# Kernel optimization log

Measured on AMD Instinct MI355X. Metric: run time of the kernel, lower is better.

## Reference

```python
import jax, jax.numpy as jnp
import numpy as np

B, K, D, H, NIRREPS = 1024, 16, 1024, 16, 16  # batch, seq_len(=group n), input_dim, heads, n_irreps
HD = D // H


def setup_inputs() -> dict:
    key = jax.random.key(0)
    ks = jax.random.split(key, 10)
    s = 1.0 / np.sqrt(D)
    return {
        "x": jax.random.normal(ks[0], (B, K, D), jnp.float32),
        "projectors": jax.random.normal(ks[1], (NIRREPS, K, K), jnp.float32) * 0.25,
        "Wq": jax.random.normal(ks[2], (D, D), jnp.float32) * s,
        "bq": jnp.zeros((D,), jnp.float32),
        "Wk": jax.random.normal(ks[3], (D, D), jnp.float32) * s,
        "bk": jnp.zeros((D,), jnp.float32),
        "Wv": jax.random.normal(ks[4], (D, D), jnp.float32) * s,
        "bv": jnp.zeros((D,), jnp.float32),
        "Wo": jax.random.normal(ks[5], (D, D), jnp.float32) * s,
        "bo": jnp.zeros((D,), jnp.float32),
    }


def reference(x, projectors, Wq, bq, Wk, bk, Wv, bv, Wo, bo):
    b, k, d = x.shape
    hd = d // H
    # QKV projections -> [b, H, k, hd]
    def heads(t):
        return t.reshape(b, k, H, hd).transpose(0, 2, 1, 3)
    Q = heads(x @ Wq + bq)
    Kt = heads(x @ Wk + bk)
    V = heads(x @ Wv + bv)
    scale = jnp.asarray(1.0 / np.sqrt(hd), x.dtype)

    # Per-irrep: project Q/K/V along the seq axis with P, run masked-free softmax
    # attention on tiny k x k scores, accumulate over irreps (eval mode, no dropout).
    def body(acc, P):
        Qp = jnp.einsum('ij,bhjd->bhid', P, Q)
        Kp = jnp.einsum('ij,bhjd->bhid', P, Kt)
        Vp = jnp.einsum('ij,bhjd->bhid', P, V)
        scores = jnp.einsum('bhid,bhjd->bhij', Qp, Kp) * scale
        w = jax.nn.softmax(scores, axis=-1)
        return acc + jnp.einsum('bhij,bhjd->bhid', w, Vp), None

    total, _ = jax.lax.scan(body, jnp.zeros_like(V), projectors)
    # merge heads -> [b, k, d], then output projection
    out = total.transpose(0, 2, 1, 3).reshape(b, k, d) @ Wo + bo
    return out
```

## Files before the change

### kernel.cpp

```cpp
#include <hip/hip_runtime.h>


typedef unsigned short u16;
typedef unsigned int u32;
typedef __attribute__((ext_vector_type(8))) __bf16 bf16x8;
typedef __attribute__((ext_vector_type(4))) float f32x4;
typedef __attribute__((ext_vector_type(4))) u32 u32x4;
typedef __attribute__((ext_vector_type(4))) u16 u16x4;
typedef __attribute__((address_space(1))) void gvoid;
typedef __attribute__((address_space(3))) void svoid;

#define MFMA16(a, b, c) __builtin_amdgcn_mfma_f32_16x16x32_bf16(a, b, c, 0, 0, 0)

__device__ __forceinline__ u16 f2bf(float f) {
  u32 u = __builtin_bit_cast(u32, f);
  return (u16)((u + 0x7fffu + ((u >> 16) & 1u)) >> 16);
}
__device__ __forceinline__ float bf2f(u16 h) {
  u32 u = ((u32)h) << 16;
  return __builtin_bit_cast(float, u);
}
__device__ __forceinline__ bf16x8 ld_frag(const u16* p) {
  u32x4 v = *reinterpret_cast<const u32x4*>(p);
  return __builtin_bit_cast(bf16x8, v);
}
__device__ __forceinline__ bf16x8 ld_frag_lo(const u16* p, int lane) {
  u32x4 v = {0u, 0u, 0u, 0u};
  if (lane < 32) v = *reinterpret_cast<const u32x4*>(p);
  return __builtin_bit_cast(bf16x8, v);
}
__device__ __forceinline__ void async16(const u16* g, u16* l) {
  __builtin_amdgcn_global_load_lds((gvoid*)g, (svoid*)l, 16, 0, 0);
}
__device__ __forceinline__ void lds_fence() {
  asm volatile("s_waitcnt lgkmcnt(0)" ::: "memory");
}

__global__ __launch_bounds__(256) void detect_dtype(const u32* __restrict__ x,
                                                    int* __restrict__ flag) {
  const int tid = threadIdx.x;
  int cnt = 0;
  for (int i = tid; i < 16384; i += 256) {
    const u32 e = (x[i] >> 23) & 0xffu;
    cnt += (e >= 64u && e <= 191u) ? 1 : 0;
  }
  __shared__ int sred[4];
  for (int o = 32; o; o >>= 1) cnt += __shfl_down(cnt, o);
  if ((tid & 63) == 0) sred[tid >> 6] = cnt;
  __syncthreads();
  if (tid == 0)
    flag[0] = (sred[0] + sred[1] + sred[2] + sred[3] > 8192) ? 1 : 0;
}

__global__ __launch_bounds__(256) void convert_bf16(const void* __restrict__ src,
                                                    u16* __restrict__ dst, int n,
                                                    const int* __restrict__ flag) {
  const int isf32 = *flag;
  const int base = (blockIdx.x * 256 + threadIdx.x) * 8;
  if (base >= n) return;
  if (isf32) {
    const float* s = (const float*)src;
#pragma unroll
    for (int j = 0; j < 8; ++j) dst[base + j] = f2bf(s[base + j]);
  } else {
    const u16* s = (const u16*)src;
#pragma unroll
    for (int j = 0; j < 8; ++j) dst[base + j] = s[base + j];
  }
}

__global__ __launch_bounds__(256) void transpose_conv(const void* __restrict__ src,
                                                      u16* __restrict__ dst,
                                                      const int* __restrict__ flag) {
  __shared__ u16 tile[32][33];
  const int isf32 = *flag;
  const int tx = threadIdx.x & 31;
  const int ty = (threadIdx.x >> 5) * 4;
  const int bx = blockIdx.x * 32;
  const int by = blockIdx.y * 32;
#pragma unroll
  for (int r = 0; r < 4; ++r) {
    const int idx = (by + ty + r) * 1024 + bx + tx;
    tile[ty + r][tx] = isf32 ? f2bf(((const float*)src)[idx]) : ((const u16*)src)[idx];
  }
  __syncthreads();
#pragma unroll
  for (int r = 0; r < 4; ++r)
    dst[(bx + ty + r) * 1024 + by + tx] = tile[tx][ty + r];
}

template <int MODE>
__global__ __launch_bounds__(256) void gemm_kernel(
    const u16* __restrict__ X, const u16* __restrict__ Wt,
    const u16* __restrict__ b0, const u16* __restrict__ b1, const u16* __restrict__ b2,
    void* __restrict__ o0, u16* __restrict__ o1, u16* __restrict__ o2,
    const int* __restrict__ flag) {
  __shared__ alignas(16) u16 As[128 * 32];
  __shared__ alignas(16) u16 Bs[128 * 32];
  const int tid = threadIdx.x;
  const int wave = tid >> 6, lane = tid & 63;
  const int m0 = blockIdx.y * 128, n0 = blockIdx.x * 128;
  const int wm = (wave >> 1) * 64, wn = (wave & 1) * 64;
  const int fr = lane & 15, fq = lane >> 4;

  f32x4 acc[4][4] = {};

  const int s0 = tid, s1 = 256 + tid;
  const u16* gA0 = X + (m0 + (s0 >> 2)) * 1024 + (s0 & 3) * 8;
  const u16* gA1 = X + (m0 + (s1 >> 2)) * 1024 + (s1 & 3) * 8;
  const u16* gB0 = Wt + (n0 + (s0 >> 2)) * 1024 + (s0 & 3) * 8;
  const u16* gB1 = Wt + (n0 + (s1 >> 2)) * 1024 + (s1 & 3) * 8;
  u16* lA0 = As + wave * 64 * 8;
  u16* lA1 = As + (256 + wave * 64) * 8;
  u16* lB0 = Bs + wave * 64 * 8;
  u16* lB1 = Bs + (256 + wave * 64) * 8;
  const u16* aRd = As + (wm + fr) * 32 + fq * 8;
  const u16* bRd = Bs + (wn + fr) * 32 + fq * 8;

  for (int kb = 0; kb < 32; ++kb) {
    const int ko = kb * 32;
    if (kb) __syncthreads();
    async16(gA0 + ko, lA0);
    async16(gA1 + ko, lA1);
    async16(gB0 + ko, lB0);
    async16(gB1 + ko, lB1);
    __syncthreads();
    bf16x8 af[4], bfr[4];
#pragma unroll
    for (int t = 0; t < 4; ++t) af[t] = ld_frag(aRd + t * 16 * 32);
#pragma unroll
    for (int t = 0; t < 4; ++t) bfr[t] = ld_frag(bRd + t * 16 * 32);
#pragma unroll
    for (int i = 0; i < 4; ++i)
#pragma unroll
      for (int j = 0; j < 4; ++j) acc[i][j] = MFMA16(af[i], bfr[j], acc[i][j]);
  }

  const int c = fr, g = fq;
  if (MODE == 0) {
    const int q = n0 >> 10;
    const int nb = (n0 & 1023) + wn;
    const u16* bp = (q == 0) ? b0 : ((q == 1) ? b1 : b2);
    u16* q0 = (u16*)o0;
#pragma unroll
    for (int tm = 0; tm < 4; ++tm) {
      const int mbase = m0 + wm + tm * 16;
      const int bidx = mbase >> 4;
#pragma unroll
      for (int tn = 0; tn < 4; ++tn) {
        const int nl = nb + tn * 16 + c;
        const int h = nl >> 6, d = nl & 63;
        const float bias = bf2f(bp[nl]);
        const int bh = bidx * 16 + h;
        if (q == 2) {
          u16x4 pk;
#pragma unroll
          for (int r = 0; r < 4; ++r) pk[r] = f2bf(acc[tm][tn][r] + bias);
          *reinterpret_cast<u16x4*>(&o2[(bh * 64 + d) * 16 + g * 4]) = pk;
        } else {
          u16* dstq = (q == 0) ? q0 : o1;
#pragma unroll
          for (int r = 0; r < 4; ++r) {
            const int j = g * 4 + r;
            dstq[(bh * 16 + j) * 64 + d] = f2bf(acc[tm][tn][r] + bias);
          }
        }
      }
    }
  } else {
    const int isf32 = *flag;
#pragma unroll
    for (int tm = 0; tm < 4; ++tm) {
      const int m = m0 + wm + tm * 16 + g * 4;
#pragma unroll
      for (int tn = 0; tn < 4; ++tn) {
        const int n = n0 + wn + tn * 16 + c;
        const float bias = bf2f(b0[n]);
        if (isf32) {
#pragma unroll
          for (int r = 0; r < 4; ++r)
            ((float*)o0)[(m + r) * 1024 + n] = acc[tm][tn][r] + bias;
        } else {
#pragma unroll
          for (int r = 0; r < 4; ++r)
            ((u16*)o0)[(m + r) * 1024 + n] = f2bf(acc[tm][tn][r] + bias);
        }
      }
    }
  }
}

__global__ __launch_bounds__(256) void attn_kernel(
    const u16* __restrict__ Qb, const u16* __restrict__ Kb, const u16* __restrict__ Vt,
    const u16* __restrict__ P, u16* __restrict__ Tb) {
  __shared__ alignas(16) u16 Pl[4096];
  __shared__ alignas(16) u16 Ptl[4096];
  __shared__ alignas(16) u16 STl[4][16 * 24];
  __shared__ alignas(16) u16 CVl[4][4][16 * 24];

  const int tid = threadIdx.x;
#pragma unroll
  for (int i = 0; i < 16; ++i) {
    const int idx = i * 256 + tid;
    const u16 v = P[idx];
    Pl[idx] = v;
    const int p = idx >> 8, rc = idx & 255, rr = rc >> 4, cc = rc & 15;
    Ptl[(p << 8) + (cc << 4) + rr] = v;
  }
  __syncthreads();

  const int wave = tid >> 6, lane = tid & 63;
  const int bh = blockIdx.x * 4 + wave;
  const int fr = lane & 15, fq = lane >> 4;
  const int c = fr, g = fq;
  u16* ST = STl[wave];

  const u16* qb = Qb + bh * 1024;
  const u16* kb = Kb + bh * 1024;
  const u16* vb = Vt + bh * 1024;

  const bf16x8 qf0 = ld_frag(qb + fr * 64 + fq * 8);
  const bf16x8 qf1 = ld_frag(qb + fr * 64 + 32 + fq * 8);
  const bf16x8 kf0 = ld_frag(kb + fr * 64 + fq * 8);
  const bf16x8 kf1 = ld_frag(kb + fr * 64 + 32 + fq * 8);
  f32x4 S = {0.f, 0.f, 0.f, 0.f};
  S = MFMA16(qf0, kf0, S);
  S = MFMA16(qf1, kf1, S);
  const float scale = 0.125f;

#pragma unroll
  for (int r = 0; r < 4; ++r) ST[c * 24 + g * 4 + r] = f2bf(S[r] * scale);
  lds_fence();
  const bf16x8 sf = ld_frag_lo(ST + fr * 24 + fq * 8, lane);

  f32x4 Macc = {0.f, 0.f, 0.f, 0.f};
  for (int pg = 0; pg < 4; ++pg) {
    const int pbase = pg * 4;
    bf16x8 pa[4];
    f32x4 Ap[4];
#pragma unroll
    for (int q = 0; q < 4; ++q)
      pa[q] = ld_frag_lo(Pl + ((pbase + q) << 8) + fr * 16 + fq * 8, lane);
#pragma unroll
    for (int q = 0; q < 4; ++q) {
      f32x4 z = {0.f, 0.f, 0.f, 0.f};
      Ap[q] = MFMA16(pa[q], sf, z);
    }
#pragma unroll
    for (int q = 0; q < 4; ++q)
#pragma unroll
      for (int r = 0; r < 4; ++r)
        CVl[wave][q][(g * 4 + r) * 24 + c] = f2bf(Ap[q][r]);
    lds_fence();
    bf16x8 aa[4];
#pragma unroll
    for (int q = 0; q < 4; ++q)
      aa[q] = ld_frag_lo(CVl[wave][q] + fr * 24 + fq * 8, lane);
    f32x4 Bp[4];
#pragma unroll
    for (int q = 0; q < 4; ++q) {
      f32x4 z = {0.f, 0.f, 0.f, 0.f};
      Bp[q] = MFMA16(aa[q], pa[q], z);
    }
    float w[4][4];
#pragma unroll
    for (int q = 0; q < 4; ++q)
#pragma unroll
      for (int r = 0; r < 4; ++r) {
        const float e = __expf(Bp[q][r]);
        float sm = e;
        sm += __shfl_xor(sm, 1);
        sm += __shfl_xor(sm, 2);
        sm += __shfl_xor(sm, 4);
        sm += __shfl_xor(sm, 8);
        w[q][r] = e / sm;
      }
    lds_fence();
#pragma unroll
    for (int q = 0; q < 4; ++q)
#pragma unroll
      for (int r = 0; r < 4; ++r)
        CVl[wave][q][(g * 4 + r) * 24 + c] = f2bf(w[q][r]);
    lds_fence();
#pragma unroll
    for (int q = 0; q < 4; ++q) {
      const bf16x8 wa = ld_frag_lo(CVl[wave][q] + fr * 24 + fq * 8, lane);
      const bf16x8 pb = ld_frag_lo(Ptl + ((pbase + q) << 8) + fr * 16 + fq * 8, lane);
      Macc = MFMA16(wa, pb, Macc);
    }
    lds_fence();
  }

#pragma unroll
  for (int r = 0; r < 4; ++r) CVl[wave][0][(g * 4 + r) * 24 + c] = f2bf(Macc[r]);
  lds_fence();
  const bf16x8 ma = ld_frag_lo(CVl[wave][0] + fr * 24 + fq * 8, lane);

  const int b = bh >> 4, h = bh & 15;
  u16* outp = Tb + (b * 16) * 1024 + h * 64;
#pragma unroll
  for (int dt = 0; dt < 4; ++dt) {
    const bf16x8 vf = ld_frag_lo(vb + (dt * 16 + fr) * 16 + fq * 8, lane);
    f32x4 o = {0.f, 0.f, 0.f, 0.f};
    o = MFMA16(ma, vf, o);
#pragma unroll
    for (int r = 0; r < 4; ++r)
      outp[(g * 4 + r) * 1024 + dt * 16 + c] = f2bf(o[r]);
  }
}

extern "C" void kernel_launch(void* const* d_in, const int* in_sizes, int n_in,
                              void* d_out, int out_size, void* d_ws, size_t ws_size,
                              hipStream_t stream) {
  const void* x = d_in[0];
  const void* proj = d_in[1];
  const void* Wq = d_in[2];
  const void* bq = d_in[3];
  const void* Wk = d_in[4];
  const void* bk = d_in[5];
  const void* Wv = d_in[6];
  const void* bv = d_in[7];
  const void* Wo = d_in[8];
  const void* bo = d_in[9];

  char* ws = (char*)d_ws;
  int* flag = (int*)ws;          ws += 256;
  u16* bqc  = (u16*)ws;          ws += 1024 * 2;
  u16* bkc  = (u16*)ws;          ws += 1024 * 2;
  u16* bvc  = (u16*)ws;          ws += 1024 * 2;
  u16* boc  = (u16*)ws;          ws += 1024 * 2;
  u16* pjc  = (u16*)ws;          ws += 4096 * 2;
  u16* WtQKV = (u16*)ws;         ws += (size_t)3072 * 1024 * 2;
  u16* WtO   = (u16*)ws;         ws += (size_t)1024 * 1024 * 2;
  u16* Xb    = (u16*)ws;         ws += (size_t)16384 * 1024 * 2;
  u16* Qbuf  = (u16*)ws;         ws += (size_t)16384 * 1024 * 2;
  u16* Kbuf  = (u16*)ws;         ws += (size_t)16384 * 1024 * 2;
  u16* Vtb   = (u16*)ws;         ws += (size_t)16384 * 1024 * 2;
  u16* Tbuf  = (u16*)ws;         ws += (size_t)16384 * 1024 * 2;

  detect_dtype<<<1, 256, 0, stream>>>((const u32*)x, flag);

  convert_bf16<<<8192, 256, 0, stream>>>(x, Xb, 16777216, flag);
  convert_bf16<<<1, 256, 0, stream>>>(bq, bqc, 1024, flag);
  convert_bf16<<<1, 256, 0, stream>>>(bk, bkc, 1024, flag);
  convert_bf16<<<1, 256, 0, stream>>>(bv, bvc, 1024, flag);
  convert_bf16<<<1, 256, 0, stream>>>(bo, boc, 1024, flag);
  convert_bf16<<<2, 256, 0, stream>>>(proj, pjc, 4096, flag);

  const dim3 tg(32, 32);
  transpose_conv<<<tg, 256, 0, stream>>>(Wq, WtQKV, flag);
  transpose_conv<<<tg, 256, 0, stream>>>(Wk, WtQKV + 1024 * 1024, flag);
  transpose_conv<<<tg, 256, 0, stream>>>(Wv, WtQKV + 2 * 1024 * 1024, flag);
  transpose_conv<<<tg, 256, 0, stream>>>(Wo, WtO, flag);

  gemm_kernel<0><<<dim3(24, 128), 256, 0, stream>>>(Xb, WtQKV, bqc, bkc, bvc,
                                                    Qbuf, Kbuf, Vtb, nullptr);
  attn_kernel<<<4096, 256, 0, stream>>>(Qbuf, Kbuf, Vtb, pjc, Tbuf);
  gemm_kernel<1><<<dim3(8, 128), 256, 0, stream>>>(Tbuf, WtO, boc, nullptr, nullptr,
                                                   d_out, nullptr, nullptr, flag);
}
```

Before: 438.5 us.

## Move attention fragments through registers via shuffles and merge setup kernels

The attention kernel no longer stages scores, projected scores and softmax weights through LDS. Instead it reformats MFMA accumulators into input fragments with cross-lane shuffles (c2frag), processes one irrep per iteration and uses transposed MFMA operand orders so the softmax row sum needs only two shuffles. The output is stored as packed 4-element vectors. The host side also fuses the small conversions and dtype detection into one kernel, vectorizes the x conversion and merges the four weight transposes into one launch, cutting launch overhead. The risk is the extra shuffle cost per fragment conversion and subtle layout mistakes in the transposed formulation.

```diff
diff --git a/kernel.cpp b/kernel.cpp
--- a/kernel.cpp
+++ b/kernel.cpp
@@ -7,6 +7,7 @@
 typedef __attribute__((ext_vector_type(4))) float f32x4;
 typedef __attribute__((ext_vector_type(4))) u32 u32x4;
 typedef __attribute__((ext_vector_type(4))) u16 u16x4;
+typedef __attribute__((ext_vector_type(4))) float float4v;
 typedef __attribute__((address_space(1))) void gvoid;
 typedef __attribute__((address_space(3))) void svoid;
 
@@ -32,47 +33,79 @@
 __device__ __forceinline__ void async16(const u16* g, u16* l) {
   __builtin_amdgcn_global_load_lds((gvoid*)g, (svoid*)l, 16, 0, 0);
 }
-__device__ __forceinline__ void lds_fence() {
-  asm volatile("s_waitcnt lgkmcnt(0)" ::: "memory");
-}
-
-__global__ __launch_bounds__(256) void detect_dtype(const u32* __restrict__ x,
-                                                    int* __restrict__ flag) {
+
+__device__ __forceinline__ bf16x8 c2frag(f32x4 v, int lane) {
+  const u32 p01 = ((u32)f2bf(v[1]) << 16) | (u32)f2bf(v[0]);
+  const u32 p23 = ((u32)f2bf(v[3]) << 16) | (u32)f2bf(v[2]);
+  const int base = (lane & 15) + ((lane & 16) << 1);
+  u32x4 o;
+  o[0] = (u32)__shfl((int)p01, base);
+  o[1] = (u32)__shfl((int)p23, base);
+  o[2] = (u32)__shfl((int)p01, base + 16);
+  o[3] = (u32)__shfl((int)p23, base + 16);
+  if (lane >= 32) o = (u32x4){0u, 0u, 0u, 0u};
+  return __builtin_bit_cast(bf16x8, o);
+}
+
+__global__ __launch_bounds__(256) void setup_small(
+    const void* __restrict__ x, const void* __restrict__ proj,
+    const void* __restrict__ bq, const void* __restrict__ bk,
+    const void* __restrict__ bv, const void* __restrict__ bo,
+    int* __restrict__ flag, u16* __restrict__ pjc, u16* __restrict__ bqc,
+    u16* __restrict__ bkc, u16* __restrict__ bvc, u16* __restrict__ boc) {
   const int tid = threadIdx.x;
   int cnt = 0;
+  const u32* xw = (const u32*)x;
   for (int i = tid; i < 16384; i += 256) {
-    const u32 e = (x[i] >> 23) & 0xffu;
+    const u32 e = (xw[i] >> 23) & 0xffu;
     cnt += (e >= 64u && e <= 191u) ? 1 : 0;
   }
   __shared__ int sred[4];
   for (int o = 32; o; o >>= 1) cnt += __shfl_down(cnt, o);
   if ((tid & 63) == 0) sred[tid >> 6] = cnt;
+  __shared__ int sflag;
   __syncthreads();
-  if (tid == 0)
-    flag[0] = (sred[0] + sred[1] + sred[2] + sred[3] > 8192) ? 1 : 0;
-}
-
-__global__ __launch_bounds__(256) void convert_bf16(const void* __restrict__ src,
-                                                    u16* __restrict__ dst, int n,
-                                                    const int* __restrict__ flag) {
-  const int isf32 = *flag;
-  const int base = (blockIdx.x * 256 + threadIdx.x) * 8;
-  if (base >= n) return;
-  if (isf32) {
-    const float* s = (const float*)src;
-#pragma unroll
-    for (int j = 0; j < 8; ++j) dst[base + j] = f2bf(s[base + j]);
+  if (tid == 0) {
+    const int f = (sred[0] + sred[1] + sred[2] + sred[3] > 8192) ? 1 : 0;
+    sflag = f;
+    flag[0] = f;
+  }
+  __syncthreads();
+  const int isf32 = sflag;
+  const void* srcs[5] = {proj, bq, bk, bv, bo};
+  u16* dsts[5] = {pjc, bqc, bkc, bvc, boc};
+  const int ns[5] = {4096, 1024, 1024, 1024, 1024};
+#pragma unroll
+  for (int t = 0; t < 5; ++t) {
+    for (int i = tid; i < ns[t]; i += 256)
+      dsts[t][i] = isf32 ? f2bf(((const float*)srcs[t])[i]) : ((const u16*)srcs[t])[i];
+  }
+}
+
+__global__ __launch_bounds__(256) void convert_x(const void* __restrict__ src,
+                                                 u16* __restrict__ dst,
+                                                 const int* __restrict__ flag) {
+  const int i4 = blockIdx.x * 256 + threadIdx.x;
+  if (*flag) {
+    const float4v v = ((const float4v*)src)[i4];
+    u16x4 o;
+#pragma unroll
+    for (int j = 0; j < 4; ++j) o[j] = f2bf(v[j]);
+    ((u16x4*)dst)[i4] = o;
   } else {
-    const u16* s = (const u16*)src;
-#pragma unroll
-    for (int j = 0; j < 8; ++j) dst[base + j] = s[base + j];
-  }
-}
-
-__global__ __launch_bounds__(256) void transpose_conv(const void* __restrict__ src,
-                                                      u16* __restrict__ dst,
-                                                      const int* __restrict__ flag) {
+    ((u16x4*)dst)[i4] = ((const u16x4*)src)[i4];
+  }
+}
+
+__global__ __launch_bounds__(256) void transpose_conv(
+    const void* __restrict__ w0, const void* __restrict__ w1,
+    const void* __restrict__ w2, const void* __restrict__ w3,
+    u16* __restrict__ d0, u16* __restrict__ d1, u16* __restrict__ d2,
+    u16* __restrict__ d3, const int* __restrict__ flag) {
   __shared__ u16 tile[32][33];
+  const int z = blockIdx.z;
+  const void* src = (z == 0) ? w0 : (z == 1) ? w1 : (z == 2) ? w2 : w3;
+  u16* dst = (z == 0) ? d0 : (z == 1) ? d1 : (z == 2) ? d2 : d3;
   const int isf32 = *flag;
   const int tx = threadIdx.x & 31;
   const int ty = (threadIdx.x >> 5) * 4;
@@ -195,9 +228,6 @@
     const u16* __restrict__ P, u16* __restrict__ Tb) {
   __shared__ alignas(16) u16 Pl[4096];
   __shared__ alignas(16) u16 Ptl[4096];
-  __shared__ alignas(16) u16 STl[4][16 * 24];
-  __shared__ alignas(16) u16 CVl[4][4][16 * 24];
-
   const int tid = threadIdx.x;
 #pragma unroll
   for (int i = 0; i < 16; ++i) {
@@ -212,8 +242,6 @@
   const int wave = tid >> 6, lane = tid & 63;
   const int bh = blockIdx.x * 4 + wave;
   const int fr = lane & 15, fq = lane >> 4;
-  const int c = fr, g = fq;
-  u16* ST = STl[wave];
 
   const u16* qb = Qb + bh * 1024;
   const u16* kb = Kb + bh * 1024;
@@ -226,86 +254,46 @@
   f32x4 S = {0.f, 0.f, 0.f, 0.f};
   S = MFMA16(qf0, kf0, S);
   S = MFMA16(qf1, kf1, S);
-  const float scale = 0.125f;
-
-#pragma unroll
-  for (int r = 0; r < 4; ++r) ST[c * 24 + g * 4 + r] = f2bf(S[r] * scale);
-  lds_fence();
-  const bf16x8 sf = ld_frag_lo(ST + fr * 24 + fq * 8, lane);
-
-  f32x4 Macc = {0.f, 0.f, 0.f, 0.f};
-  for (int pg = 0; pg < 4; ++pg) {
-    const int pbase = pg * 4;
-    bf16x8 pa[4];
-    f32x4 Ap[4];
-#pragma unroll
-    for (int q = 0; q < 4; ++q)
-      pa[q] = ld_frag_lo(Pl + ((pbase + q) << 8) + fr * 16 + fq * 8, lane);
-#pragma unroll
-    for (int q = 0; q < 4; ++q) {
-      f32x4 z = {0.f, 0.f, 0.f, 0.f};
-      Ap[q] = MFMA16(pa[q], sf, z);
+#pragma unroll
+  for (int r = 0; r < 4; ++r) S[r] *= 0.125f;
+  const bf16x8 St = c2frag(S, lane);
+
+  f32x4 Mt = {0.f, 0.f, 0.f, 0.f};
+#pragma unroll 4
+  for (int p = 0; p < 16; ++p) {
+    const bf16x8 pl = ld_frag_lo(Pl + (p << 8) + fr * 16 + fq * 8, lane);
+    const bf16x8 pt = ld_frag_lo(Ptl + (p << 8) + fr * 16 + fq * 8, lane);
+    f32x4 z = {0.f, 0.f, 0.f, 0.f};
+    const f32x4 ApT = MFMA16(St, pl, z);
+    const f32x4 BpT = MFMA16(pl, c2frag(ApT, lane), z);
+    float e[4], s = 0.f;
+#pragma unroll
+    for (int r = 0; r < 4; ++r) {
+      e[r] = __expf(BpT[r]);
+      s += e[r];
     }
-#pragma unroll
-    for (int q = 0; q < 4; ++q)
-#pragma unroll
-      for (int r = 0; r < 4; ++r)
-        CVl[wave][q][(g * 4 + r) * 24 + c] = f2bf(Ap[q][r]);
-    lds_fence();
-    bf16x8 aa[4];
-#pragma unroll
-    for (int q = 0; q < 4; ++q)
-      aa[q] = ld_frag_lo(CVl[wave][q] + fr * 24 + fq * 8, lane);
-    f32x4 Bp[4];
-#pragma unroll
-    for (int q = 0; q < 4; ++q) {
-      f32x4 z = {0.f, 0.f, 0.f, 0.f};
-      Bp[q] = MFMA16(aa[q], pa[q], z);
-    }
-    float w[4][4];
-#pragma unroll
-    for (int q = 0; q < 4; ++q)
-#pragma unroll
-      for (int r = 0; r < 4; ++r) {
-        const float e = __expf(Bp[q][r]);
-        float sm = e;
-        sm += __shfl_xor(sm, 1);
-        sm += __shfl_xor(sm, 2);
-        sm += __shfl_xor(sm, 4);
-        sm += __shfl_xor(sm, 8);
-        w[q][r] = e / sm;
-      }
-    lds_fence();
-#pragma unroll
-    for (int q = 0; q < 4; ++q)
-#pragma unroll
-      for (int r = 0; r < 4; ++r)
-        CVl[wave][q][(g * 4 + r) * 24 + c] = f2bf(w[q][r]);
-    lds_fence();
-#pragma unroll
-    for (int q = 0; q < 4; ++q) {
-      const bf16x8 wa = ld_frag_lo(CVl[wave][q] + fr * 24 + fq * 8, lane);
-      const bf16x8 pb = ld_frag_lo(Ptl + ((pbase + q) << 8) + fr * 16 + fq * 8, lane);
-      Macc = MFMA16(wa, pb, Macc);
-    }
-    lds_fence();
-  }
-
-#pragma unroll
-  for (int r = 0; r < 4; ++r) CVl[wave][0][(g * 4 + r) * 24 + c] = f2bf(Macc[r]);
-  lds_fence();
-  const bf16x8 ma = ld_frag_lo(CVl[wave][0] + fr * 24 + fq * 8, lane);
+    s += __shfl_xor(s, 16);
+    s += __shfl_xor(s, 32);
+    const float rs = __frcp_rn(s);
+    f32x4 w;
+#pragma unroll
+    for (int r = 0; r < 4; ++r) w[r] = e[r] * rs;
+    Mt = MFMA16(pt, c2frag(w, lane), Mt);
+  }
+
+  const bf16x8 mb = c2frag(Mt, lane);
 
   const int b = bh >> 4, h = bh & 15;
-  u16* outp = Tb + (b * 16) * 1024 + h * 64;
+  u16* outp = Tb + (b * 16 + fr) * 1024 + h * 64;
 #pragma unroll
   for (int dt = 0; dt < 4; ++dt) {
     const bf16x8 vf = ld_frag_lo(vb + (dt * 16 + fr) * 16 + fq * 8, lane);
-    f32x4 o = {0.f, 0.f, 0.f, 0.f};
-    o = MFMA16(ma, vf, o);
-#pragma unroll
-    for (int r = 0; r < 4; ++r)
-      outp[(g * 4 + r) * 1024 + dt * 16 + c] = f2bf(o[r]);
+    f32x4 z = {0.f, 0.f, 0.f, 0.f};
+    const f32x4 ot = MFMA16(vf, mb, z);
+    u16x4 pk;
+#pragma unroll
+    for (int r = 0; r < 4; ++r) pk[r] = f2bf(ot[r]);
+    *reinterpret_cast<u16x4*>(&outp[dt * 16 + fq * 4]) = pk;
   }
 }
 
@@ -338,20 +326,11 @@
   u16* Vtb   = (u16*)ws;         ws += (size_t)16384 * 1024 * 2;
   u16* Tbuf  = (u16*)ws;         ws += (size_t)16384 * 1024 * 2;
 
-  detect_dtype<<<1, 256, 0, stream>>>((const u32*)x, flag);
-
-  convert_bf16<<<8192, 256, 0, stream>>>(x, Xb, 16777216, flag);
-  convert_bf16<<<1, 256, 0, stream>>>(bq, bqc, 1024, flag);
-  convert_bf16<<<1, 256, 0, stream>>>(bk, bkc, 1024, flag);
-  convert_bf16<<<1, 256, 0, stream>>>(bv, bvc, 1024, flag);
-  convert_bf16<<<1, 256, 0, stream>>>(bo, boc, 1024, flag);
-  convert_bf16<<<2, 256, 0, stream>>>(proj, pjc, 4096, flag);
-
-  const dim3 tg(32, 32);
-  transpose_conv<<<tg, 256, 0, stream>>>(Wq, WtQKV, flag);
-  transpose_conv<<<tg, 256, 0, stream>>>(Wk, WtQKV + 1024 * 1024, flag);
-  transpose_conv<<<tg, 256, 0, stream>>>(Wv, WtQKV + 2 * 1024 * 1024, flag);
-  transpose_conv<<<tg, 256, 0, stream>>>(Wo, WtO, flag);
+  setup_small<<<1, 256, 0, stream>>>(x, proj, bq, bk, bv, bo, flag, pjc, bqc, bkc,
+                                     bvc, boc);
+  convert_x<<<16384, 256, 0, stream>>>(x, Xb, flag);
+  transpose_conv<<<dim3(32, 32, 4), 256, 0, stream>>>(
+      Wq, Wk, Wv, Wo, WtQKV, WtQKV + 1024 * 1024, WtQKV + 2 * 1024 * 1024, WtO, flag);
 
   gemm_kernel<0><<<dim3(24, 128), 256, 0, stream>>>(Xb, WtQKV, bqc, bkc, bvc,
                                                     Qbuf, Kbuf, Vtb, nullptr);
```

Result: faster. 405.9 us (-7.4%).
